# Kernel tuning notes

Measured on AMD Instinct MI355X. Metric: run time of the kernel, lower is better.

Reference implementation:

```python
import jax, jax.numpy as jnp
import numpy as np

B, C, H, W = 2, 512, 64, 64
G = 32          # GroupNorm groups
EPS = 1e-6


def setup_inputs() -> dict:
    key = jax.random.key(0)
    ks = jax.random.split(key, 10)
    s = 1.0 / np.sqrt(C)
    return {
        "x": jax.random.normal(ks[0], (B, C, H, W), dtype=jnp.float32),
        "gn_w": jnp.ones((C,), jnp.float32),
        "gn_b": jnp.zeros((C,), jnp.float32),
        "wq": jax.random.normal(ks[1], (C, C), jnp.float32) * s,
        "bq": jnp.zeros((C,), jnp.float32),
        "wk": jax.random.normal(ks[2], (C, C), jnp.float32) * s,
        "bk": jnp.zeros((C,), jnp.float32),
        "wv": jax.random.normal(ks[3], (C, C), jnp.float32) * s,
        "bv": jnp.zeros((C,), jnp.float32),
        "wo": jax.random.normal(ks[4], (C, C), jnp.float32) * s,
        "bo": jnp.zeros((C,), jnp.float32),
    }


def reference(x, gn_w, gn_b, wq, bq, wk, bk, wv, bv, wo, bo):
    b, c, h, w = x.shape
    n = h * w
    # GroupNorm(32, eps=1e-6, affine)
    xg = x.reshape(b, G, c // G, h, w)
    mu = xg.mean(axis=(2, 3, 4), keepdims=True)
    var = ((xg - mu) ** 2).mean(axis=(2, 3, 4), keepdims=True)
    hn = ((xg - mu) * jax.lax.rsqrt(var + EPS)).reshape(b, c, h, w)
    hn = hn * gn_w[None, :, None, None] + gn_b[None, :, None, None]
    # 1x1 convs == per-pixel linear over channels; tokens: b n c
    hf = hn.reshape(b, c, n)
    q = jnp.einsum('oc,bcn->bno', wq, hf) + bq  # [b, n, c]
    k = jnp.einsum('oc,bcn->bno', wk, hf) + bk
    v = jnp.einsum('oc,bcn->bno', wv, hf) + bv
    scale = jnp.asarray(c, x.dtype) ** -0.5
    att = jax.nn.softmax(jnp.einsum('bic,bjc->bij', q, k) * scale, axis=-1)
    o = jnp.einsum('bij,bjc->bic', att, v)      # [b, n, c]
    out = jnp.einsum('oc,bnc->bno', wo, o) + bo # proj_out
    return x + out.transpose(0, 2, 1).reshape(b, c, h, w)
```

## Files before the change

### kernel.cpp

```cpp
#include <hip/hip_runtime.h>
#include <hip/hip_bf16.h>


typedef float f32x4 __attribute__((ext_vector_type(4)));
typedef __bf16 bf16x8 __attribute__((ext_vector_type(8)));

typedef const __attribute__((address_space(1))) unsigned char* gas_p;
typedef __attribute__((address_space(3))) unsigned char* las_p;

__device__ __forceinline__ void gload_lds16(const void* g, void* l) {
  __builtin_amdgcn_global_load_lds((gas_p)g, (las_p)l, 16, 0, 0);
}

__global__ __launch_bounds__(256) void gn_stats_k(const float* __restrict__ x,
                                                  float* __restrict__ stats) {
  int bg = blockIdx.x;
  const float4* p = (const float4*)(x + (size_t)bg * 65536);
  float s = 0.f, s2 = 0.f;
  for (int i = threadIdx.x; i < 16384; i += 256) {
    float4 v = p[i];
    s  += v.x + v.y + v.z + v.w;
    s2 += v.x * v.x + v.y * v.y + v.z * v.z + v.w * v.w;
  }
#pragma unroll
  for (int off = 32; off > 0; off >>= 1) {
    s  += __shfl_xor(s, off);
    s2 += __shfl_xor(s2, off);
  }
  __shared__ float rs[4], rs2[4];
  int wid = threadIdx.x >> 6, lane = threadIdx.x & 63;
  if (lane == 0) { rs[wid] = s; rs2[wid] = s2; }
  __syncthreads();
  if (threadIdx.x == 0) {
    float S  = rs[0] + rs[1] + rs[2] + rs[3];
    float S2 = rs2[0] + rs2[1] + rs2[2] + rs2[3];
    float mean = S * (1.f / 65536.f);
    float var  = S2 * (1.f / 65536.f) - mean * mean;
    stats[bg * 2]     = mean;
    stats[bg * 2 + 1] = rsqrtf(var + 1e-6f);
  }
}

__global__ __launch_bounds__(256) void gn_apply_k(const float* __restrict__ x,
                                                  const float* __restrict__ stats,
                                                  const float* __restrict__ gw,
                                                  const float* __restrict__ gb,
                                                  __hip_bfloat16* __restrict__ hf) {
  int c0 = blockIdx.x * 64, n0 = blockIdx.y * 64, b = blockIdx.z;
  __shared__ float tile[64][65];
  int tx = threadIdx.x & 63, ty = threadIdx.x >> 6;
  const float* xb = x + ((size_t)(b * 512 + c0)) * 4096 + n0;
#pragma unroll
  for (int i = 0; i < 64; i += 4) {
    int cl = i + ty;
    int c  = c0 + cl;
    float mean = stats[(b * 32 + (c >> 4)) * 2];
    float rstd = stats[(b * 32 + (c >> 4)) * 2 + 1];
    float v = xb[(size_t)cl * 4096 + tx];
    tile[cl][tx] = (v - mean) * rstd * gw[c] + gb[c];
  }
  __syncthreads();
  __hip_bfloat16* o = hf + ((size_t)(b * 4096 + n0)) * 512 + c0;
#pragma unroll
  for (int i = 0; i < 64; i += 4) {
    int nl = i + ty;
    o[(size_t)nl * 512 + tx] = __float2bfloat16(tile[tx][nl]);
  }
}

__global__ __launch_bounds__(256) void cvt_k(const float* __restrict__ w,
                                             __hip_bfloat16* __restrict__ o, int n) {
  int i = blockIdx.x * 256 + threadIdx.x;
  if (i < n) o[i] = __float2bfloat16(w[i]);
}

__global__ __launch_bounds__(256) void bcat_k(const float* __restrict__ bq,
                                              const float* __restrict__ bk,
                                              float* __restrict__ bqk) {
  int i = blockIdx.x * 256 + threadIdx.x;
  if (i < 512) bqk[i] = bq[i];
  else if (i < 1024) bqk[i] = bk[i - 512];
}

__global__ __launch_bounds__(256, 4) void qkv_k(
    const __hip_bfloat16* __restrict__ hf, const __hip_bfloat16* __restrict__ wqk,
    const __hip_bfloat16* __restrict__ wv, const float* __restrict__ bqk,
    const float* __restrict__ bv, __hip_bfloat16* __restrict__ qk,
    __hip_bfloat16* __restrict__ vT) {
  bool isV = blockIdx.x >= 8;
  int m0 = isV ? (blockIdx.x - 8) * 128 : blockIdx.y * 128;
  int n0 = isV ? blockIdx.y * 128 : blockIdx.x * 128;
  const __hip_bfloat16* A  = isV ? wv : hf;
  const __hip_bfloat16* Bm = isV ? hf : wqk;

  __shared__ __hip_bfloat16 As[2 * 4096];
  __shared__ __hip_bfloat16 Bs[2 * 4096];

  int tid  = threadIdx.x;
  int wvx  = tid >> 6, lane = tid & 63;
  int wr   = (wvx >> 1) * 64, wc = (wvx & 1) * 64;
  int quad = lane >> 4, l16 = lane & 15;

  int srow = wvx * 32 + (lane >> 2);
  int scol = (lane & 3) * 8;
  const __hip_bfloat16* gA0 = A  + (size_t)(m0 + srow) * 512 + scol;
  const __hip_bfloat16* gA1 = gA0 + (size_t)16 * 512;
  const __hip_bfloat16* gB0 = Bm + (size_t)(n0 + srow) * 512 + scol;
  const __hip_bfloat16* gB1 = gB0 + (size_t)16 * 512;

  auto stage = [&](int kk, int bsel) {
    int lb = bsel * 4096 + wvx * 1024;
    gload_lds16(gA0 + kk, &As[lb]);
    gload_lds16(gA1 + kk, &As[lb + 512]);
    gload_lds16(gB0 + kk, &Bs[lb]);
    gload_lds16(gB1 + kk, &Bs[lb + 512]);
  };

  f32x4 acc[4][4] = {};
  stage(0, 0);
  for (int kt = 0; kt < 16; kt++) {
    __syncthreads();
    if (kt + 1 < 16) stage((kt + 1) << 5, (kt + 1) & 1);
    const __hip_bfloat16* Ab = &As[(kt & 1) * 4096];
    const __hip_bfloat16* Bb = &Bs[(kt & 1) * 4096];
    bf16x8 af[4], bfr[4];
#pragma unroll
    for (int i = 0; i < 4; i++)
      af[i] = *(const bf16x8*)&Ab[(wr + i * 16 + l16) * 32 + quad * 8];
#pragma unroll
    for (int j = 0; j < 4; j++)
      bfr[j] = *(const bf16x8*)&Bb[(wc + j * 16 + l16) * 32 + quad * 8];
#pragma unroll
    for (int i = 0; i < 4; i++)
#pragma unroll
      for (int j = 0; j < 4; j++)
        acc[i][j] = __builtin_amdgcn_mfma_f32_16x16x32_bf16(af[i], bfr[j],
                                                            acc[i][j], 0, 0, 0);
  }
#pragma unroll
  for (int i = 0; i < 4; i++)
#pragma unroll
    for (int j = 0; j < 4; j++)
#pragma unroll
      for (int r = 0; r < 4; r++) {
        int m = m0 + wr + i * 16 + quad * 4 + r;
        int n = n0 + wc + j * 16 + l16;
        float v = acc[i][j][r];
        if (!isV) {
          qk[(size_t)m * 1024 + n] = __float2bfloat16(v + bqk[n]);
        } else {
          int b = n >> 12, t = n & 4095;
          vT[((size_t)(b * 512 + m)) * 4096 + t] = __float2bfloat16(v + bv[m]);
        }
      }
}

template <int MODE>
__global__ __launch_bounds__(256, 4) void gemm_bt_k(
    const __hip_bfloat16* __restrict__ A, const __hip_bfloat16* __restrict__ Bm,
    void* __restrict__ Cout, const float* __restrict__ bias,
    const float* __restrict__ resid, int Kc, int lda, int ldb, int ldc,
    float scale, long sAz, long sBz, long sCz, int kspl) {
  int bx, by, bz;
  if (MODE == 3) {
    int f = blockIdx.x;
    int xcd = f & 7, s = f >> 3;
    bx = s & 3;
    int g = xcd + 8 * (s >> 2);
    by = g & 31;
    bz = g >> 5;
  } else {
    bx = blockIdx.x; by = blockIdx.y; bz = blockIdx.z;
  }
  int bb = bz / kspl, ks = bz - bb * kspl;
  A  += (size_t)bb * sAz + (size_t)ks * Kc;
  Bm += (size_t)bb * sBz + (size_t)ks * Kc;
  size_t cbase = (size_t)bz * sCz;
  int m0 = by * 128, n0 = bx * 128;

  __shared__ __hip_bfloat16 As[2 * 4096];
  __shared__ __hip_bfloat16 Bs[2 * 4096];

  int tid  = threadIdx.x;
  int wv   = tid >> 6, lane = tid & 63;
  int wr   = (wv >> 1) * 64, wc = (wv & 1) * 64;
  int quad = lane >> 4, l16 = lane & 15;

  int srow = wv * 32 + (lane >> 2);
  int scol = (lane & 3) * 8;
  const __hip_bfloat16* gA0 = A  + (size_t)(m0 + srow) * lda + scol;
  const __hip_bfloat16* gA1 = gA0 + (size_t)16 * lda;
  const __hip_bfloat16* gB0 = Bm + (size_t)(n0 + srow) * ldb + scol;
  const __hip_bfloat16* gB1 = gB0 + (size_t)16 * ldb;

  auto stage = [&](int kk, int bsel) {
    int lb = bsel * 4096 + wv * 1024;
    gload_lds16(gA0 + kk, &As[lb]);
    gload_lds16(gA1 + kk, &As[lb + 512]);
    gload_lds16(gB0 + kk, &Bs[lb]);
    gload_lds16(gB1 + kk, &Bs[lb + 512]);
  };

  int KT = Kc >> 5;
  f32x4 acc[4][4] = {};
  stage(0, 0);
  for (int kt = 0; kt < KT; kt++) {
    __syncthreads();
    if (kt + 1 < KT) stage((kt + 1) << 5, (kt + 1) & 1);
    const __hip_bfloat16* Ab = &As[(kt & 1) * 4096];
    const __hip_bfloat16* Bb = &Bs[(kt & 1) * 4096];
    bf16x8 af[4], bfr[4];
#pragma unroll
    for (int i = 0; i < 4; i++)
      af[i] = *(const bf16x8*)&Ab[(wr + i * 16 + l16) * 32 + quad * 8];
#pragma unroll
    for (int j = 0; j < 4; j++)
      bfr[j] = *(const bf16x8*)&Bb[(wc + j * 16 + l16) * 32 + quad * 8];
#pragma unroll
    for (int i = 0; i < 4; i++)
#pragma unroll
      for (int j = 0; j < 4; j++)
        acc[i][j] = __builtin_amdgcn_mfma_f32_16x16x32_bf16(af[i], bfr[j],
                                                            acc[i][j], 0, 0, 0);
  }

#pragma unroll
  for (int i = 0; i < 4; i++)
#pragma unroll
    for (int j = 0; j < 4; j++)
#pragma unroll
      for (int r = 0; r < 4; r++) {
        int m = m0 + wr + i * 16 + quad * 4 + r;
        int n = n0 + wc + j * 16 + l16;
        float v = acc[i][j][r];
        size_t idx = cbase + (size_t)m * ldc + n;
        if (MODE == 2) {
          ((__hip_bfloat16*)Cout)[idx] = __float2bfloat16(v * scale);
        } else if (MODE == 3) {
          ((__hip_bfloat16*)Cout)[idx] = __float2bfloat16(v);
        } else {
          ((float*)Cout)[idx] = resid[idx] + v + bias[m];
        }
      }
}

__global__ __launch_bounds__(256) void softmax_k(__hip_bfloat16* __restrict__ S) {
  size_t row = blockIdx.x;
  bf16x8* s = (bf16x8*)(S + row * 4096);
  bf16x8 r0 = s[threadIdx.x];
  bf16x8 r1 = s[threadIdx.x + 256];
  float v[16];
#pragma unroll
  for (int l = 0; l < 8; l++) { v[l] = (float)r0[l]; v[8 + l] = (float)r1[l]; }
  float m = -1e30f;
#pragma unroll
  for (int i = 0; i < 16; i++) m = fmaxf(m, v[i]);
#pragma unroll
  for (int off = 32; off > 0; off >>= 1) m = fmaxf(m, __shfl_xor(m, off));
  __shared__ float red[4], red2[4];
  int wid = threadIdx.x >> 6, lane = threadIdx.x & 63;
  if (lane == 0) red[wid] = m;
  __syncthreads();
  m = fmaxf(fmaxf(red[0], red[1]), fmaxf(red[2], red[3]));
  float sum = 0.f;
#pragma unroll
  for (int i = 0; i < 16; i++) {
    v[i] = __expf(v[i] - m);
    sum += v[i];
  }
#pragma unroll
  for (int off = 32; off > 0; off >>= 1) sum += __shfl_xor(sum, off);
  if (lane == 0) red2[wid] = sum;
  __syncthreads();
  sum = red2[0] + red2[1] + red2[2] + red2[3];
  float inv = 1.f / sum;
  bf16x8 o0, o1;
#pragma unroll
  for (int l = 0; l < 8; l++) {
    o0[l] = (__bf16)(v[l] * inv);
    o1[l] = (__bf16)(v[8 + l] * inv);
  }
  s[threadIdx.x] = o0;
  s[threadIdx.x + 256] = o1;
}

__global__ __launch_bounds__(256) void reduce_k(const __hip_bfloat16* __restrict__ part,
                                                __hip_bfloat16* __restrict__ obuf) {
  size_t i8 = (size_t)blockIdx.x * 256 + threadIdx.x;
  size_t perb = (size_t)4096 * 512 / 8;
  size_t b = i8 / perb, r = i8 - b * perb;
  float acc[8] = {};
#pragma unroll
  for (int ks = 0; ks < 4; ks++) {
    bf16x8 v = ((const bf16x8*)part)[(b * 4 + ks) * perb + r];
#pragma unroll
    for (int l = 0; l < 8; l++) acc[l] += (float)v[l];
  }
  bf16x8 o;
#pragma unroll
  for (int l = 0; l < 8; l++) o[l] = (__bf16)acc[l];
  ((bf16x8*)obuf)[b * perb + r] = o;
}

extern "C" void kernel_launch(void* const* d_in, const int* in_sizes, int n_in,
                              void* d_out, int out_size, void* d_ws,
                              size_t ws_size, hipStream_t stream) {
  const float* xp  = (const float*)d_in[0];
  const float* gwp = (const float*)d_in[1];
  const float* gbp = (const float*)d_in[2];
  const float* wqp = (const float*)d_in[3];
  const float* bqp = (const float*)d_in[4];
  const float* wkp = (const float*)d_in[5];
  const float* bkp = (const float*)d_in[6];
  const float* wvp = (const float*)d_in[7];
  const float* bvp = (const float*)d_in[8];
  const float* wop = (const float*)d_in[9];
  const float* bop = (const float*)d_in[10];
  float* outp = (float*)d_out;

  char* w = (char*)d_ws;
  size_t off = 0;
  auto alloc = [&](size_t bytes) {
    void* p = w + off;
    off += (bytes + 255) & ~(size_t)255;
    return p;
  };
  float* stats         = (float*)alloc(64 * 2 * sizeof(float));
  __hip_bfloat16* hf   = (__hip_bfloat16*)alloc((size_t)2 * 4096 * 512 * 2);
  __hip_bfloat16* wqkb = (__hip_bfloat16*)alloc((size_t)1024 * 512 * 2);
  __hip_bfloat16* wvb  = (__hip_bfloat16*)alloc((size_t)512 * 512 * 2);
  __hip_bfloat16* wob  = (__hip_bfloat16*)alloc((size_t)512 * 512 * 2);
  float* bqk           = (float*)alloc(1024 * sizeof(float));
  __hip_bfloat16* qk   = (__hip_bfloat16*)alloc((size_t)2 * 4096 * 1024 * 2);
  __hip_bfloat16* vT   = (__hip_bfloat16*)alloc((size_t)2 * 512 * 4096 * 2);
  __hip_bfloat16* obuf = (__hip_bfloat16*)alloc((size_t)2 * 4096 * 512 * 2);
  __hip_bfloat16* part = (__hip_bfloat16*)alloc((size_t)8 * 4096 * 512 * 2);
  __hip_bfloat16* Sbuf = (__hip_bfloat16*)alloc((size_t)2 * 4096 * 4096 * 2);

  const int NW = 262144;
  const int CVG = (NW + 255) / 256;

  gn_stats_k<<<64, 256, 0, stream>>>(xp, stats);
  gn_apply_k<<<dim3(8, 64, 2), 256, 0, stream>>>(xp, stats, gwp, gbp, hf);
  cvt_k<<<CVG, 256, 0, stream>>>(wqp, wqkb, NW);
  cvt_k<<<CVG, 256, 0, stream>>>(wkp, wqkb + NW, NW);
  cvt_k<<<CVG, 256, 0, stream>>>(wvp, wvb, NW);
  cvt_k<<<CVG, 256, 0, stream>>>(wop, wob, NW);
  bcat_k<<<4, 256, 0, stream>>>(bqp, bkp, bqk);

  qkv_k<<<dim3(12, 64, 1), 256, 0, stream>>>(hf, wqkb, wvb, bqk, bvp, qk, vT);

  gemm_bt_k<2><<<dim3(32, 32, 2), 256, 0, stream>>>(
      qk, qk + 512, Sbuf, nullptr, nullptr, 512, 1024, 1024, 4096,
      0.044194173824159216f, (long)4096 * 1024, (long)4096 * 1024,
      (long)4096 * 4096, 1);

  softmax_k<<<8192, 256, 0, stream>>>(Sbuf);

  gemm_bt_k<3><<<dim3(1024, 1, 1), 256, 0, stream>>>(
      Sbuf, vT, part, nullptr, nullptr, 1024, 4096, 4096, 512, 1.f,
      (long)4096 * 4096, (long)512 * 4096, (long)4096 * 512, 4);

  reduce_k<<<2048, 256, 0, stream>>>(part, obuf);

  gemm_bt_k<6><<<dim3(32, 4, 2), 256, 0, stream>>>(
      wob, obuf, outp, bop, xp, 512, 512, 512, 4096, 1.f,
      0, (long)4096 * 512, (long)512 * 4096, 1);
}
```

Measured before the change: 292.1 us.

## Fuse softmax into QK and PV GEMM epilogues and stage stores through LDS

Drops the standalone softmax kernel. The QK^T GEMM now writes exp(scaled scores) and accumulates per-row sums with atomics, and the PV GEMM scales its partial outputs by the reciprocal row sum. All GEMM epilogues, including qkv, go through an LDS tile so global stores are coalesced 16-byte vector writes. This removes a full read and write pass over the 64MB score matrix. It gives up the max-subtraction, so exp can overflow if scores are large, and the sum is taken over bf16-rounded values.

```diff
diff --git a/kernel.cpp b/kernel.cpp
--- a/kernel.cpp
+++ b/kernel.cpp
@@ -80,6 +80,11 @@
   int i = blockIdx.x * 256 + threadIdx.x;
   if (i < 512) bqk[i] = bq[i];
   else if (i < 1024) bqk[i] = bk[i - 512];
+}
+
+__global__ __launch_bounds__(256) void zero_k(float* __restrict__ p, int n) {
+  int i = blockIdx.x * 256 + threadIdx.x;
+  if (i < n) p[i] = 0.f;
 }
 
 __global__ __launch_bounds__(256, 4) void qkv_k(
@@ -93,8 +98,10 @@
   const __hip_bfloat16* A  = isV ? wv : hf;
   const __hip_bfloat16* Bm = isV ? hf : wqk;
 
-  __shared__ __hip_bfloat16 As[2 * 4096];
-  __shared__ __hip_bfloat16 Bs[2 * 4096];
+  __shared__ __align__(16) unsigned char smem[34816];
+  __hip_bfloat16* As  = (__hip_bfloat16*)smem;
+  __hip_bfloat16* Bs  = As + 8192;
+  __hip_bfloat16* epi = (__hip_bfloat16*)smem;
 
   int tid  = threadIdx.x;
   int wvx  = tid >> 6, lane = tid & 63;
@@ -137,30 +144,54 @@
         acc[i][j] = __builtin_amdgcn_mfma_f32_16x16x32_bf16(af[i], bfr[j],
                                                             acc[i][j], 0, 0, 0);
   }
+
+  float bj[4], bm[4][4];
+  if (!isV) {
+#pragma unroll
+    for (int j = 0; j < 4; j++) bj[j] = bqk[n0 + wc + j * 16 + l16];
+  } else {
+#pragma unroll
+    for (int i = 0; i < 4; i++)
+#pragma unroll
+      for (int r = 0; r < 4; r++)
+        bm[i][r] = bv[m0 + wr + i * 16 + quad * 4 + r];
+  }
+  __syncthreads();
 #pragma unroll
   for (int i = 0; i < 4; i++)
 #pragma unroll
     for (int j = 0; j < 4; j++)
 #pragma unroll
       for (int r = 0; r < 4; r++) {
-        int m = m0 + wr + i * 16 + quad * 4 + r;
-        int n = n0 + wc + j * 16 + l16;
-        float v = acc[i][j][r];
-        if (!isV) {
-          qk[(size_t)m * 1024 + n] = __float2bfloat16(v + bqk[n]);
-        } else {
-          int b = n >> 12, t = n & 4095;
-          vT[((size_t)(b * 512 + m)) * 4096 + t] = __float2bfloat16(v + bv[m]);
-        }
+        int ml = wr + i * 16 + quad * 4 + r;
+        int nl = wc + j * 16 + l16;
+        float v = acc[i][j][r] + (isV ? bm[i][r] : bj[j]);
+        epi[ml * 136 + nl] = __float2bfloat16(v);
       }
+  __syncthreads();
+  int mr = tid >> 1, h = tid & 1;
+  const __hip_bfloat16* rowp = &epi[mr * 136 + h * 64];
+  if (!isV) {
+    __hip_bfloat16* o = qk + (size_t)(m0 + mr) * 1024 + n0 + h * 64;
+#pragma unroll
+    for (int c = 0; c < 8; c++)
+      *(uint4*)(o + c * 8) = *(const uint4*)(rowp + c * 8);
+  } else {
+    int b = (n0 + h * 64) >> 12, t = (n0 + h * 64) & 4095;
+    __hip_bfloat16* o = vT + ((size_t)(b * 512 + m0 + mr)) * 4096 + t;
+#pragma unroll
+    for (int c = 0; c < 8; c++)
+      *(uint4*)(o + c * 8) = *(const uint4*)(rowp + c * 8);
+  }
 }
 
 template <int MODE>
 __global__ __launch_bounds__(256, 4) void gemm_bt_k(
     const __hip_bfloat16* __restrict__ A, const __hip_bfloat16* __restrict__ Bm,
     void* __restrict__ Cout, const float* __restrict__ bias,
-    const float* __restrict__ resid, int Kc, int lda, int ldb, int ldc,
-    float scale, long sAz, long sBz, long sCz, int kspl) {
+    const float* __restrict__ resid, float* __restrict__ rowsum, int Kc,
+    int lda, int ldb, int ldc, float scale, long sAz, long sBz, long sCz,
+    int kspl) {
   int bx, by, bz;
   if (MODE == 3) {
     int f = blockIdx.x;
@@ -178,8 +209,10 @@
   size_t cbase = (size_t)bz * sCz;
   int m0 = by * 128, n0 = bx * 128;
 
-  __shared__ __hip_bfloat16 As[2 * 4096];
-  __shared__ __hip_bfloat16 Bs[2 * 4096];
+  __shared__ __align__(16) unsigned char smem[34816];
+  __hip_bfloat16* As  = (__hip_bfloat16*)smem;
+  __hip_bfloat16* Bs  = As + 8192;
+  __hip_bfloat16* epi = (__hip_bfloat16*)smem;
 
   int tid  = threadIdx.x;
   int wv   = tid >> 6, lane = tid & 63;
@@ -224,64 +257,74 @@
                                                             acc[i][j], 0, 0, 0);
   }
 
+  float pre[4][4];
+  if (MODE == 3) {
+#pragma unroll
+    for (int i = 0; i < 4; i++)
+#pragma unroll
+      for (int r = 0; r < 4; r++)
+        pre[i][r] = 1.f / rowsum[bb * 4096 + m0 + wr + i * 16 + quad * 4 + r];
+  } else if (MODE == 6) {
+#pragma unroll
+    for (int i = 0; i < 4; i++)
+#pragma unroll
+      for (int r = 0; r < 4; r++)
+        pre[i][r] = bias[m0 + wr + i * 16 + quad * 4 + r];
+  }
+  __syncthreads();
 #pragma unroll
   for (int i = 0; i < 4; i++)
 #pragma unroll
     for (int j = 0; j < 4; j++)
 #pragma unroll
       for (int r = 0; r < 4; r++) {
-        int m = m0 + wr + i * 16 + quad * 4 + r;
-        int n = n0 + wc + j * 16 + l16;
+        int ml = wr + i * 16 + quad * 4 + r;
+        int nl = wc + j * 16 + l16;
         float v = acc[i][j][r];
-        size_t idx = cbase + (size_t)m * ldc + n;
-        if (MODE == 2) {
-          ((__hip_bfloat16*)Cout)[idx] = __float2bfloat16(v * scale);
-        } else if (MODE == 3) {
-          ((__hip_bfloat16*)Cout)[idx] = __float2bfloat16(v);
-        } else {
-          ((float*)Cout)[idx] = resid[idx] + v + bias[m];
-        }
+        if (MODE == 2) v = __expf(v * scale);
+        else if (MODE == 3) v *= pre[i][r];
+        else v += pre[i][r];
+        epi[ml * 136 + nl] = __float2bfloat16(v);
       }
-}
-
-__global__ __launch_bounds__(256) void softmax_k(__hip_bfloat16* __restrict__ S) {
-  size_t row = blockIdx.x;
-  bf16x8* s = (bf16x8*)(S + row * 4096);
-  bf16x8 r0 = s[threadIdx.x];
-  bf16x8 r1 = s[threadIdx.x + 256];
-  float v[16];
-#pragma unroll
-  for (int l = 0; l < 8; l++) { v[l] = (float)r0[l]; v[8 + l] = (float)r1[l]; }
-  float m = -1e30f;
-#pragma unroll
-  for (int i = 0; i < 16; i++) m = fmaxf(m, v[i]);
-#pragma unroll
-  for (int off = 32; off > 0; off >>= 1) m = fmaxf(m, __shfl_xor(m, off));
-  __shared__ float red[4], red2[4];
-  int wid = threadIdx.x >> 6, lane = threadIdx.x & 63;
-  if (lane == 0) red[wid] = m;
-  __syncthreads();
-  m = fmaxf(fmaxf(red[0], red[1]), fmaxf(red[2], red[3]));
-  float sum = 0.f;
-#pragma unroll
-  for (int i = 0; i < 16; i++) {
-    v[i] = __expf(v[i] - m);
-    sum += v[i];
-  }
-#pragma unroll
-  for (int off = 32; off > 0; off >>= 1) sum += __shfl_xor(sum, off);
-  if (lane == 0) red2[wid] = sum;
-  __syncthreads();
-  sum = red2[0] + red2[1] + red2[2] + red2[3];
-  float inv = 1.f / sum;
-  bf16x8 o0, o1;
-#pragma unroll
-  for (int l = 0; l < 8; l++) {
-    o0[l] = (__bf16)(v[l] * inv);
-    o1[l] = (__bf16)(v[8 + l] * inv);
-  }
-  s[threadIdx.x] = o0;
-  s[threadIdx.x + 256] = o1;
+  __syncthreads();
+  int mr = tid >> 1, h = tid & 1;
+  const __hip_bfloat16* rowp = &epi[mr * 136 + h * 64];
+  int gm = m0 + mr;
+  size_t obase = cbase + (size_t)gm * ldc + n0 + h * 64;
+  if (MODE == 2) {
+    float s = 0.f;
+    __hip_bfloat16* o = (__hip_bfloat16*)Cout + obase;
+#pragma unroll
+    for (int c = 0; c < 8; c++) {
+      bf16x8 val = *(const bf16x8*)(rowp + c * 8);
+#pragma unroll
+      for (int l = 0; l < 8; l++) s += (float)val[l];
+      *(uint4*)(o + c * 8) = *(const uint4*)&val;
+    }
+    s += __shfl_xor(s, 1);
+    if (h == 0) atomicAdd(&rowsum[bb * 4096 + gm], s);
+  } else if (MODE == 3) {
+    __hip_bfloat16* o = (__hip_bfloat16*)Cout + obase;
+#pragma unroll
+    for (int c = 0; c < 8; c++)
+      *(uint4*)(o + c * 8) = *(const uint4*)(rowp + c * 8);
+  } else {
+    float* o = (float*)Cout;
+#pragma unroll
+    for (int c = 0; c < 8; c++) {
+      bf16x8 val = *(const bf16x8*)(rowp + c * 8);
+      size_t idx = obase + c * 8;
+      float4 r0 = *(const float4*)&resid[idx];
+      float4 r1 = *(const float4*)&resid[idx + 4];
+      float4 o0, o1;
+      o0.x = r0.x + (float)val[0]; o0.y = r0.y + (float)val[1];
+      o0.z = r0.z + (float)val[2]; o0.w = r0.w + (float)val[3];
+      o1.x = r1.x + (float)val[4]; o1.y = r1.y + (float)val[5];
+      o1.z = r1.z + (float)val[6]; o1.w = r1.w + (float)val[7];
+      *(float4*)&o[idx] = o0;
+      *(float4*)&o[idx + 4] = o1;
+    }
+  }
 }
 
 __global__ __launch_bounds__(256) void reduce_k(const __hip_bfloat16* __restrict__ part,
@@ -331,6 +374,7 @@
   __hip_bfloat16* wvb  = (__hip_bfloat16*)alloc((size_t)512 * 512 * 2);
   __hip_bfloat16* wob  = (__hip_bfloat16*)alloc((size_t)512 * 512 * 2);
   float* bqk           = (float*)alloc(1024 * sizeof(float));
+  float* rowsum        = (float*)alloc(8192 * sizeof(float));
   __hip_bfloat16* qk   = (__hip_bfloat16*)alloc((size_t)2 * 4096 * 1024 * 2);
   __hip_bfloat16* vT   = (__hip_bfloat16*)alloc((size_t)2 * 512 * 4096 * 2);
   __hip_bfloat16* obuf = (__hip_bfloat16*)alloc((size_t)2 * 4096 * 512 * 2);
@@ -347,23 +391,22 @@
   cvt_k<<<CVG, 256, 0, stream>>>(wvp, wvb, NW);
   cvt_k<<<CVG, 256, 0, stream>>>(wop, wob, NW);
   bcat_k<<<4, 256, 0, stream>>>(bqp, bkp, bqk);
+  zero_k<<<32, 256, 0, stream>>>(rowsum, 8192);
 
   qkv_k<<<dim3(12, 64, 1), 256, 0, stream>>>(hf, wqkb, wvb, bqk, bvp, qk, vT);
 
   gemm_bt_k<2><<<dim3(32, 32, 2), 256, 0, stream>>>(
-      qk, qk + 512, Sbuf, nullptr, nullptr, 512, 1024, 1024, 4096,
+      qk, qk + 512, Sbuf, nullptr, nullptr, rowsum, 512, 1024, 1024, 4096,
       0.044194173824159216f, (long)4096 * 1024, (long)4096 * 1024,
       (long)4096 * 4096, 1);
 
-  softmax_k<<<8192, 256, 0, stream>>>(Sbuf);
-
   gemm_bt_k<3><<<dim3(1024, 1, 1), 256, 0, stream>>>(
-      Sbuf, vT, part, nullptr, nullptr, 1024, 4096, 4096, 512, 1.f,
+      Sbuf, vT, part, nullptr, nullptr, rowsum, 1024, 4096, 4096, 512, 1.f,
       (long)4096 * 4096, (long)512 * 4096, (long)4096 * 512, 4);
 
   reduce_k<<<2048, 256, 0, stream>>>(part, obuf);
 
   gemm_bt_k<6><<<dim3(32, 4, 2), 256, 0, stream>>>(
-      wob, obuf, outp, bop, xp, 512, 512, 512, 4096, 1.f,
+      wob, obuf, outp, bop, xp, nullptr, 512, 512, 512, 4096, 1.f,
       0, (long)4096 * 512, (long)512 * 4096, 1);
 }
```

After: 290.3 us. No clear change (-0.6%).
